# Optimization experiments

Measured on AMD Instinct MI355X. Metric: run time of the kernel, lower is better.

## Reference

```python
import jax, jax.numpy as jnp
import numpy as np

B, S, D, H = 2, 2048, 1024, 16
DK = D // H

def setup_inputs() -> dict:
    key = jax.random.key(0)
    ks = jax.random.split(key, 12)
    s = 1.0 / np.sqrt(D)
    return {
        "q": jax.random.normal(ks[0], (B, S, D), jnp.float32),
        "k": jax.random.normal(ks[1], (B, S, D), jnp.float32),
        "v": jax.random.normal(ks[2], (B, S, D), jnp.float32),
        "mask": jnp.ones((1, 1, S, S), jnp.int32),
        "Wq": jax.random.normal(ks[3], (D, D), jnp.float32) * s,
        "bq": jnp.zeros((D,), jnp.float32),
        "Wk": jax.random.normal(ks[4], (D, D), jnp.float32) * s,
        "bk": jnp.zeros((D,), jnp.float32),
        "Wv": jax.random.normal(ks[5], (D, D), jnp.float32) * s,
        "bv": jnp.zeros((D,), jnp.float32),
        "Wo": jax.random.normal(ks[6], (D, D), jnp.float32) * s,
        "bo": jnp.zeros((D,), jnp.float32),
    }

def reference(q, k, v, mask, Wq, bq, Wk, bk, Wv, bv, Wo, bo):
    # projections (torch Linear: x @ W^T + b)
    Q = q @ Wq.T + bq
    K = k @ Wk.T + bk
    V = v @ Wv.T + bv
    # split heads: [B,S,D] -> [B,H,S,DK]
    def split(x):
        return x.reshape(B, S, H, DK).transpose(0, 2, 1, 3)
    Qh, Kh, Vh = split(Q), split(K), split(V)
    scores = jnp.einsum('bhqd,bhkd->bhqk', Qh, Kh) / jnp.sqrt(jnp.float32(DK))
    scores = jnp.where(mask == 0, jnp.float32(-1e9), scores)
    attn = jax.nn.softmax(scores, axis=-1)  # dropout p=0.0 -> identity
    x = jnp.einsum('bhqk,bhkd->bhqd', attn, Vh)
    x = x.transpose(0, 2, 1, 3).reshape(B, S, D)
    return x @ Wo.T + bo
```

## Files before the change

### kernel.cpp

```cpp
#include <hip/hip_runtime.h>
#include <hip/hip_bf16.h>
#include <stdint.h>

#define B_    2
#define S_    2048
#define D_    1024
#define H_    16
#define NTOK  (B_ * S_)

typedef __attribute__((ext_vector_type(8))) short bf16x8;
typedef __attribute__((ext_vector_type(4))) float f32x4;
typedef __attribute__((ext_vector_type(2))) float float2v;
typedef __attribute__((ext_vector_type(2))) __bf16 bfv2;

static __device__ __forceinline__ unsigned int pkbf(float a, float b) {
    float2v fv = {a, b};
    bfv2 r = __builtin_convertvector(fv, bfv2);
    unsigned int u;
    __builtin_memcpy(&u, &r, 4);
    return u;
}

using g_cu32 = __attribute__((address_space(1))) const unsigned int;
using l_u32  = __attribute__((address_space(3))) unsigned int;
static __device__ __forceinline__ void gld16(const void* g, void* l) {
    __builtin_amdgcn_global_load_lds((g_cu32*)g, (l_u32*)l, 16, 0, 0);
}

template<int N> static __device__ __forceinline__ void wait_vm() {
    if constexpr (N == 0)      asm volatile("s_waitcnt vmcnt(0)" ::: "memory");
    else if constexpr (N == 2) asm volatile("s_waitcnt vmcnt(2)" ::: "memory");
    else if constexpr (N == 3) asm volatile("s_waitcnt vmcnt(3)" ::: "memory");
    else if constexpr (N == 4) asm volatile("s_waitcnt vmcnt(4)" ::: "memory");
}

#define QN ((size_t)NTOK * D_)
#define WN ((size_t)D_ * D_)

struct SwapT { static constexpr bool value = true; };
struct NoSwapT { static constexpr bool value = false; };

__global__ __launch_bounds__(256) void prep_kernel(
    const float* __restrict__ q, const float* __restrict__ k, const float* __restrict__ v,
    const float* __restrict__ Wq, const float* __restrict__ Wk,
    const float* __restrict__ Wv, const float* __restrict__ Wo,
    const int* __restrict__ mask,
    unsigned short* __restrict__ qb, unsigned short* __restrict__ kb,
    unsigned short* __restrict__ vb, unsigned short* __restrict__ wqb,
    unsigned short* __restrict__ wkb, unsigned short* __restrict__ wvb,
    unsigned short* __restrict__ wob, int* __restrict__ flags) {
    __shared__ int anyz;
    if (blockIdx.x < 8192) {
        size_t i = ((size_t)blockIdx.x * 256 + threadIdx.x) * 8;
        const float* s; unsigned short* d; size_t off;
        if (i < QN)          { s = q; d = qb; off = i; }
        else if (i < 2 * QN) { s = k; d = kb; off = i - QN; }
        else if (i < 3 * QN) { s = v; d = vb; off = i - 2 * QN; }
        else {
            size_t j = i - 3 * QN;
            int wi = (int)(j >> 20);
            s = (wi == 0) ? Wq : (wi == 1) ? Wk : (wi == 2) ? Wv : Wo;
            d = (wi == 0) ? wqb : (wi == 1) ? wkb : (wi == 2) ? wvb : wob;
            off = j & (WN - 1);
        }
        float4 a = *(const float4*)(s + off);
        float4 b = *(const float4*)(s + off + 4);
        uint4 pk;
        pk.x = pkbf(a.x, a.y); pk.y = pkbf(a.z, a.w);
        pk.z = pkbf(b.x, b.y); pk.w = pkbf(b.z, b.w);
        *(uint4*)(d + off) = pk;
    } else {
        if (threadIdx.x == 0) anyz = 0;
        __syncthreads();
        int bid2 = blockIdx.x - 8192;
        const int qt = bid2 >> 5, kt = bid2 & 31;
        int az = 0;
        for (int i = threadIdx.x; i < 64 * 64; i += 256) {
            int r = i >> 6, c = i & 63;
            az |= (mask[(size_t)(qt * 64 + r) * S_ + kt * 64 + c] == 0) ? 1 : 0;
        }
        if (az) atomicOr(&anyz, 1);
        __syncthreads();
        if (threadIdx.x == 0) flags[qt * 32 + kt] = anyz;
    }
}

struct GemmArgs {
    const unsigned short* A[3];
    const unsigned short* W[3];
    const float* bias[3];
    void* C[3];
    int mode[3];
    float scale[3];
};

template<int BMT>
__global__ __launch_bounds__(256, 3) void gemm_async(GemmArgs ga) {
    constexpr int AG = BMT / 16;
    constexpr int MI = BMT / 32;
    constexpr int NK = D_ / 32;
    constexpr int LOADS = (BMT == 128) ? 4 : 3;
    const int z = blockIdx.z;
    const unsigned short* __restrict__ A = ga.A[z];
    const unsigned short* __restrict__ W = ga.W[z];
    const float* __restrict__ bias = ga.bias[z];
    void* C = ga.C[z];
    const int mode = ga.mode[z];
    const float scl = ga.scale[z];

    __shared__ unsigned short As[3][AG * 512];
    __shared__ unsigned short Bs[3][8 * 512];

    const int t    = threadIdx.x;
    const int lane = t & 63;
    const int w    = t >> 6;
    const int fr   = lane & 15;
    const int kq   = lane >> 4;
    const int wrow = w >> 1, wcol = w & 1;
    const int m0 = blockIdx.x * BMT, n0 = blockIdx.y * 128;

    const int sc = lane >> 4;
    const int sr = lane & 15;

    const unsigned short* ga0;
    const unsigned short* ga1 = nullptr;
    int la0Off, la1Off = 0;
    if constexpr (BMT == 128) {
        ga0 = A + (size_t)(m0 + (2 * w) * 16 + sr) * D_ + sc * 8;
        ga1 = ga0 + 16 * D_;
        la0Off = (2 * w) * 512;
        la1Off = (2 * w + 1) * 512;
    } else {
        ga0 = A + (size_t)(m0 + w * 16 + sr) * D_ + sc * 8;
        la0Off = w * 512;
    }
    const unsigned short* gw0 = W + (size_t)(n0 + (2 * w) * 16 + sr) * D_ + sc * 8;
    const unsigned short* gw1 = gw0 + 16 * D_;
    const int lw0Off = (2 * w) * 512;
    const int lw1Off = (2 * w + 1) * 512;

    int aOff[MI], bOff[4];
#pragma unroll
    for (int mi = 0; mi < MI; ++mi) aOff[mi] = (wrow * MI + mi) * 512 + (kq * 16 + fr) * 8;
#pragma unroll
    for (int ni = 0; ni < 4; ++ni) bOff[ni] = (wcol * 4 + ni) * 512 + (kq * 16 + fr) * 8;

    f32x4 acc[MI][4];
#pragma unroll
    for (int i = 0; i < MI; ++i)
#pragma unroll
        for (int j = 0; j < 4; ++j) acc[i][j] = (f32x4)0.0f;

    auto stage = [&](int buf) {
        gld16(ga0, &As[buf][la0Off]);
        if constexpr (BMT == 128) gld16(ga1, &As[buf][la1Off]);
        gld16(gw0, &Bs[buf][lw0Off]);
        gld16(gw1, &Bs[buf][lw1Off]);
        ga0 += 32; gw0 += 32; gw1 += 32;
        if constexpr (BMT == 128) ga1 += 32;
    };

    auto kloop = [&](auto swc) {
        constexpr bool SW = decltype(swc)::value;
        auto mma_step = [&](int cur) {
            const unsigned short* Ab = As[cur];
            const unsigned short* Bb = Bs[cur];
            bf16x8 af[MI], bfr[4];
#pragma unroll
            for (int mi = 0; mi < MI; ++mi) af[mi] = *(const bf16x8*)&Ab[aOff[mi]];
#pragma unroll
            for (int ni = 0; ni < 4; ++ni) bfr[ni] = *(const bf16x8*)&Bb[bOff[ni]];
#pragma unroll
            for (int mi = 0; mi < MI; ++mi)
#pragma unroll
                for (int ni = 0; ni < 4; ++ni) {
                    if constexpr (SW)
                        acc[mi][ni] = __builtin_amdgcn_mfma_f32_16x16x32_bf16(
                            bfr[ni], af[mi], acc[mi][ni], 0, 0, 0);
                    else
                        acc[mi][ni] = __builtin_amdgcn_mfma_f32_16x16x32_bf16(
                            af[mi], bfr[ni], acc[mi][ni], 0, 0, 0);
                }
        };

        stage(0);
        stage(1);
        int cur = 0;
        for (int k0 = 0; k0 < NK - 1; ++k0) {
            __builtin_amdgcn_sched_barrier(0);
            wait_vm<LOADS>();
            __builtin_amdgcn_s_barrier();
            __builtin_amdgcn_sched_barrier(0);
            if (k0 + 2 < NK) {
                int pf = (cur >= 1) ? cur - 1 : cur + 2;
                stage(pf);
            }
            mma_step(cur);
            cur = (cur < 2) ? cur + 1 : 0;
        }
        __builtin_amdgcn_sched_barrier(0);
        wait_vm<0>();
        __builtin_amdgcn_s_barrier();
        __builtin_amdgcn_sched_barrier(0);
        mma_step(cur);
    };
    if (mode == 2) kloop(NoSwapT{}); else kloop(SwapT{});

    if (mode == 2) {
        unsigned short* Co = (unsigned short*)C;
#pragma unroll
        for (int ni = 0; ni < 4; ++ni) {
            int col = n0 + wcol * 64 + ni * 16 + fr;
            float bv = bias[col];
            int hh = col >> 6, d = col & 63;
#pragma unroll
            for (int mi = 0; mi < MI; ++mi) {
                int tok = m0 + wrow * (BMT / 2) + mi * 16 + kq * 4;
                int bb = tok >> 11, sbase = tok & (S_ - 1);
                uint2 pk;
                pk.x = pkbf((acc[mi][ni][0] + bv) * scl, (acc[mi][ni][1] + bv) * scl);
                pk.y = pkbf((acc[mi][ni][2] + bv) * scl, (acc[mi][ni][3] + bv) * scl);
                *(uint2*)(Co + ((size_t)((bb * H_ + hh) * 64 + d)) * S_ + sbase) = pk;
            }
        }
    } else if (mode == 0) {
        float* Co = (float*)C;
#pragma unroll
        for (int ni = 0; ni < 4; ++ni) {
            int nb = n0 + wcol * 64 + ni * 16 + kq * 4;
            float4 b4 = *(const float4*)&bias[nb];
#pragma unroll
            for (int mi = 0; mi < MI; ++mi) {
                int m = m0 + wrow * (BMT / 2) + mi * 16 + fr;
                float4 o4;
                o4.x = (acc[mi][ni][0] + b4.x) * scl;
                o4.y = (acc[mi][ni][1] + b4.y) * scl;
                o4.z = (acc[mi][ni][2] + b4.z) * scl;
                o4.w = (acc[mi][ni][3] + b4.w) * scl;
                *(float4*)(Co + (size_t)m * D_ + nb) = o4;
            }
        }
    } else {
        unsigned short* Co = (unsigned short*)C;
#pragma unroll
        for (int ni = 0; ni < 4; ++ni) {
            int nb = n0 + wcol * 64 + ni * 16 + kq * 4;
            float4 b4 = *(const float4*)&bias[nb];
#pragma unroll
            for (int mi = 0; mi < MI; ++mi) {
                int m = m0 + wrow * (BMT / 2) + mi * 16 + fr;
                uint2 pk;
                pk.x = pkbf((acc[mi][ni][0] + b4.x) * scl, (acc[mi][ni][1] + b4.y) * scl);
                pk.y = pkbf((acc[mi][ni][2] + b4.z) * scl, (acc[mi][ni][3] + b4.w) * scl);
                *(uint2*)(Co + (size_t)m * D_ + nb) = pk;
            }
        }
    }
}

__global__ __launch_bounds__(512, 4) void flash4(
    const unsigned short* __restrict__ Qb, const unsigned short* __restrict__ Kb,
    const unsigned short* __restrict__ Vtg, const int* __restrict__ mask,
    const int* __restrict__ flags, unsigned short* __restrict__ Xb) {
    __shared__ unsigned short Ks[3][4096];
    __shared__ unsigned short Vs[3][4096];
    __shared__ unsigned short Ps[8192];

    const int t    = threadIdx.x;
    const int lane = t & 63;
    const int w    = t >> 6;
    const int fr   = lane & 15;
    const int kq   = lane >> 4;
    const int bid = blockIdx.x;
    const int swb = ((bid & 7) << 6) | (bid >> 3);
    const int qt = swb & 15, hd = (swb >> 4) & 15, b = swb >> 8;
    const int q0 = qt * 128;
    const int swz = fr & 7;

    const unsigned short* qrow_p = Qb + (size_t)(b * S_ + q0 + w * 16 + fr) * D_ + hd * 64;
    bf16x8 qf[2];
    qf[0] = *(const bf16x8*)(qrow_p + kq * 8);
    qf[1] = *(const bf16x8*)(qrow_p + 32 + kq * 8);

    int fl = (lane < 32) ? flags[(qt * 2 + (w >> 2)) * 32 + lane] : 0;
    unsigned int fmask = (unsigned int)__ballot(fl != 0);

    const unsigned short* kptr =
        Kb + (size_t)(b * S_ + (w >> 1) * 16 + fr) * D_ + hd * 64 + (w & 1) * 32 + kq * 8;
    const unsigned short* vptr =
        Vtg + ((size_t)((b * H_ + hd) * 64 + (w >> 1) * 16 + fr)) * S_ + (w & 1) * 32 + kq * 8;

    gld16(kptr, (char*)&Ks[0][0] + w * 1024);
    gld16(vptr, (char*)&Vs[0][0] + w * 1024);
    gld16(kptr + (size_t)64 * D_, (char*)&Ks[1][0] + w * 1024);
    gld16(vptr + 64,              (char*)&Vs[1][0] + w * 1024);
    const unsigned short* kpf = kptr + (size_t)128 * D_;
    const unsigned short* vpf = vptr + 128;

    unsigned short* pswr[4];
#pragma unroll
    for (int mi = 0; mi < 4; ++mi) {
        int chunk = mi * 2 + (kq >> 1);
        pswr[mi] = &Ps[(w * 16 + fr) * 64 + ((chunk ^ swz) << 3) + ((kq & 1) << 2)];
    }
    const unsigned short* psrd[2];
#pragma unroll
    for (int kk = 0; kk < 2; ++kk) {
        int c = kk * 4 + kq;
        psrd[kk] = &Ps[(w * 16 + fr) * 64 + ((c ^ swz) << 3)];
    }

    const f32x4 zf = (f32x4)0.0f;
    f32x4 o[4];
#pragma unroll
    for (int i = 0; i < 4; ++i) o[i] = zf;
    float2v l2 = {0.0f, 0.0f};

    auto attn_step = [&](int cur, int kt) {
        f32x4 st[4];
#pragma unroll
        for (int mi = 0; mi < 4; ++mi) {
            bf16x8 a = *(const bf16x8*)&Ks[cur][mi * 1024 + (kq * 16 + fr) * 8];
            st[mi] = __builtin_amdgcn_mfma_f32_16x16x32_bf16(a, qf[0], zf, 0, 0, 0);
        }
#pragma unroll
        for (int mi = 0; mi < 4; ++mi) {
            bf16x8 a = *(const bf16x8*)&Ks[cur][mi * 1024 + ((4 + kq) * 16 + fr) * 8];
            st[mi] = __builtin_amdgcn_mfma_f32_16x16x32_bf16(a, qf[1], st[mi], 0, 0, 0);
        }

        if ((fmask >> kt) & 1u) {
#pragma unroll
            for (int mi = 0; mi < 4; ++mi) {
                int4 mv = *(const int4*)&mask[(size_t)(q0 + w * 16 + fr) * S_ + kt * 64 + mi * 16 + kq * 4];
                if (mv.x == 0) st[mi][0] = -3e8f;
                if (mv.y == 0) st[mi][1] = -3e8f;
                if (mv.z == 0) st[mi][2] = -3e8f;
                if (mv.w == 0) st[mi][3] = -3e8f;
            }
        }

#pragma unroll
        for (int mi = 0; mi < 4; ++mi) {
            float e0 = __builtin_amdgcn_exp2f(st[mi][0]);
            float e1 = __builtin_amdgcn_exp2f(st[mi][1]);
            float e2 = __builtin_amdgcn_exp2f(st[mi][2]);
            float e3 = __builtin_amdgcn_exp2f(st[mi][3]);
            l2 += (float2v){e0, e1} + (float2v){e2, e3};
            uint2 pk;
            pk.x = pkbf(e0, e1);
            pk.y = pkbf(e2, e3);
            *(uint2*)pswr[mi] = pk;
        }

#pragma unroll
        for (int kk = 0; kk < 2; ++kk) {
            bf16x8 pb = *(const bf16x8*)psrd[kk];
#pragma unroll
            for (int mi = 0; mi < 4; ++mi) {
                bf16x8 a = *(const bf16x8*)&Vs[cur][mi * 1024 + ((kk * 4 + kq) * 16 + fr) * 8];
                o[mi] = __builtin_amdgcn_mfma_f32_16x16x32_bf16(a, pb, o[mi], 0, 0, 0);
            }
        }
    };

    int cur = 0;
    for (int kt = 0; kt < 31; ++kt) {
        __builtin_amdgcn_sched_barrier(0);
        wait_vm<2>();
        __builtin_amdgcn_s_barrier();
        __builtin_amdgcn_sched_barrier(0);
        if (kt < 30) {
            int pf = (cur >= 1) ? cur - 1 : cur + 2;
            gld16(kpf, (char*)&Ks[pf][0] + w * 1024);
            gld16(vpf, (char*)&Vs[pf][0] + w * 1024);
            kpf += (size_t)64 * D_;
            vpf += 64;
        }
        attn_step(cur, kt);
        cur = (cur < 2) ? cur + 1 : 0;
    }
    __builtin_amdgcn_sched_barrier(0);
    wait_vm<0>();
    __builtin_amdgcn_s_barrier();
    __builtin_amdgcn_sched_barrier(0);
    attn_step(cur, 31);

    float l_i = l2.x + l2.y;
    l_i += __shfl_xor(l_i, 16, 64);
    l_i += __shfl_xor(l_i, 32, 64);
    float rl = 1.0f / l_i;

#pragma unroll
    for (int mi = 0; mi < 4; ++mi) {
        uint2 pk;
        pk.x = pkbf(o[mi][0] * rl, o[mi][1] * rl);
        pk.y = pkbf(o[mi][2] * rl, o[mi][3] * rl);
        *(uint2*)(Xb + (size_t)(b * S_ + q0 + w * 16 + fr) * D_ + hd * 64 + mi * 16 + kq * 4) = pk;
    }
}

extern "C" void kernel_launch(void* const* d_in, const int* in_sizes, int n_in,
                              void* d_out, int out_size, void* d_ws, size_t ws_size,
                              hipStream_t stream) {
    const float* q    = (const float*)d_in[0];
    const float* k    = (const float*)d_in[1];
    const float* v    = (const float*)d_in[2];
    const int*   mask = (const int*)d_in[3];
    const float* Wq   = (const float*)d_in[4];
    const float* bq   = (const float*)d_in[5];
    const float* Wk   = (const float*)d_in[6];
    const float* bk   = (const float*)d_in[7];
    const float* Wv   = (const float*)d_in[8];
    const float* bv   = (const float*)d_in[9];
    const float* Wo   = (const float*)d_in[10];
    const float* bo   = (const float*)d_in[11];
    float* out = (float*)d_out;

    unsigned short* qb  = (unsigned short*)d_ws;
    unsigned short* kb  = qb + QN;
    unsigned short* vb  = kb + QN;
    unsigned short* Qf  = vb + QN;
    unsigned short* Kf  = Qf + QN;
    unsigned short* Vt  = Kf + QN;
    unsigned short* wqb = Vt + QN;
    unsigned short* wkb = wqb + WN;
    unsigned short* wvb = wkb + WN;
    unsigned short* wob = wvb + WN;
    int* flags = (int*)(wob + WN);

    const float SC = 0.18033688011112042f;

    prep_kernel<<<9216, 256, 0, stream>>>(q, k, v, Wq, Wk, Wv, Wo, mask,
                                          qb, kb, vb, wqb, wkb, wvb, wob, flags);

    GemmArgs g1;
    g1.A[0] = qb;  g1.W[0] = wqb; g1.bias[0] = bq; g1.C[0] = Qf; g1.mode[0] = 1; g1.scale[0] = SC;
    g1.A[1] = kb;  g1.W[1] = wkb; g1.bias[1] = bk; g1.C[1] = Kf; g1.mode[1] = 1; g1.scale[1] = 1.0f;
    g1.A[2] = vb;  g1.W[2] = wvb; g1.bias[2] = bv; g1.C[2] = Vt; g1.mode[2] = 2; g1.scale[2] = 1.0f;
    gemm_async<128><<<dim3(NTOK / 128, D_ / 128, 3), 256, 0, stream>>>(g1);

    flash4<<<dim3((S_ / 128) * H_ * B_, 1, 1), 512, 0, stream>>>(Qf, Kf, Vt, mask, flags, Qf);

    GemmArgs g2;
    g2.A[0] = Qf; g2.W[0] = wob; g2.bias[0] = bo; g2.C[0] = out; g2.mode[0] = 0; g2.scale[0] = 1.0f;
    g2.A[1] = g2.A[2] = nullptr; g2.W[1] = g2.W[2] = nullptr;
    g2.bias[1] = g2.bias[2] = nullptr; g2.C[1] = g2.C[2] = nullptr;
    g2.mode[1] = g2.mode[2] = 0; g2.scale[1] = g2.scale[2] = 1.0f;
    gemm_async<64><<<dim3(NTOK / 64, D_ / 128, 1), 256, 0, stream>>>(g2);
}
```

Measured before the change: 260.6 us.

## Double flash query tile per block and swizzle GEMM block order across XCDs

The attention kernel now processes 256 query rows per block (two 16-row chunks per wave), so each K/V tile loaded into shared memory is reused for twice as many queries. The block count halves and the P buffer doubles, and launch bounds drop to 2 blocks per CU to allow the extra registers. The GEMMs switch to a 1D grid whose block index is remapped so neighbouring tiles land on the same XCD, aiming at better L2 locality. This trades lower occupancy and fewer blocks (256 on a large-CU part) for less K/V traffic.

```diff
diff --git a/kernel.cpp b/kernel.cpp
--- a/kernel.cpp
+++ b/kernel.cpp
@@ -100,7 +100,17 @@
     constexpr int MI = BMT / 32;
     constexpr int NK = D_ / 32;
     constexpr int LOADS = (BMT == 128) ? 4 : 3;
-    const int z = blockIdx.z;
+    constexpr int MT = NTOK / BMT;
+    constexpr int PERZ = MT * 8;
+
+    const int bid = blockIdx.x;
+    const int nb8 = (int)gridDim.x >> 3;
+    const int l = (bid & 7) * nb8 + (bid >> 3);
+    const int z = l / PERZ;
+    const int r = l % PERZ;
+    const int bx = r % MT;
+    const int by = r / MT;
+
     const unsigned short* __restrict__ A = ga.A[z];
     const unsigned short* __restrict__ W = ga.W[z];
     const float* __restrict__ bias = ga.bias[z];
@@ -117,7 +127,7 @@
     const int fr   = lane & 15;
     const int kq   = lane >> 4;
     const int wrow = w >> 1, wcol = w & 1;
-    const int m0 = blockIdx.x * BMT, n0 = blockIdx.y * 128;
+    const int m0 = bx * BMT, n0 = by * 128;
 
     const int sc = lane >> 4;
     const int sr = lane & 15;
@@ -258,13 +268,13 @@
     }
 }
 
-__global__ __launch_bounds__(512, 4) void flash4(
+__global__ __launch_bounds__(512, 2) void flash4(
     const unsigned short* __restrict__ Qb, const unsigned short* __restrict__ Kb,
     const unsigned short* __restrict__ Vtg, const int* __restrict__ mask,
     const int* __restrict__ flags, unsigned short* __restrict__ Xb) {
     __shared__ unsigned short Ks[3][4096];
     __shared__ unsigned short Vs[3][4096];
-    __shared__ unsigned short Ps[8192];
+    __shared__ unsigned short Ps[16384];
 
     const int t    = threadIdx.x;
     const int lane = t & 63;
@@ -272,18 +282,27 @@
     const int fr   = lane & 15;
     const int kq   = lane >> 4;
     const int bid = blockIdx.x;
-    const int swb = ((bid & 7) << 6) | (bid >> 3);
-    const int qt = swb & 15, hd = (swb >> 4) & 15, b = swb >> 8;
-    const int q0 = qt * 128;
+    const int swb = ((bid & 7) << 5) | (bid >> 3);
+    const int qt = swb & 7, hd = (swb >> 3) & 15, b = swb >> 7;
+    const int q0 = qt * 256;
     const int swz = fr & 7;
 
-    const unsigned short* qrow_p = Qb + (size_t)(b * S_ + q0 + w * 16 + fr) * D_ + hd * 64;
-    bf16x8 qf[2];
-    qf[0] = *(const bf16x8*)(qrow_p + kq * 8);
-    qf[1] = *(const bf16x8*)(qrow_p + 32 + kq * 8);
-
-    int fl = (lane < 32) ? flags[(qt * 2 + (w >> 2)) * 32 + lane] : 0;
-    unsigned int fmask = (unsigned int)__ballot(fl != 0);
+    bf16x8 qf[2][2];
+#pragma unroll
+    for (int qc = 0; qc < 2; ++qc) {
+        const unsigned short* qrow_p =
+            Qb + (size_t)(b * S_ + q0 + w * 32 + qc * 16 + fr) * D_ + hd * 64;
+        qf[qc][0] = *(const bf16x8*)(qrow_p + kq * 8);
+        qf[qc][1] = *(const bf16x8*)(qrow_p + 32 + kq * 8);
+    }
+
+    unsigned int fmask[2];
+#pragma unroll
+    for (int qc = 0; qc < 2; ++qc) {
+        int qt64 = qt * 4 + ((2 * w + qc) >> 2);
+        int fl = (lane < 32) ? flags[qt64 * 32 + lane] : 0;
+        fmask[qc] = (unsigned int)__ballot(fl != 0);
+    }
 
     const unsigned short* kptr =
         Kb + (size_t)(b * S_ + (w >> 1) * 16 + fr) * D_ + hd * 64 + (w & 1) * 32 + kq * 8;
@@ -297,69 +316,87 @@
     const unsigned short* kpf = kptr + (size_t)128 * D_;
     const unsigned short* vpf = vptr + 128;
 
-    unsigned short* pswr[4];
-#pragma unroll
-    for (int mi = 0; mi < 4; ++mi) {
-        int chunk = mi * 2 + (kq >> 1);
-        pswr[mi] = &Ps[(w * 16 + fr) * 64 + ((chunk ^ swz) << 3) + ((kq & 1) << 2)];
-    }
-    const unsigned short* psrd[2];
-#pragma unroll
-    for (int kk = 0; kk < 2; ++kk) {
-        int c = kk * 4 + kq;
-        psrd[kk] = &Ps[(w * 16 + fr) * 64 + ((c ^ swz) << 3)];
+    unsigned short* pswr[2][4];
+    const unsigned short* psrd[2][2];
+#pragma unroll
+    for (int qc = 0; qc < 2; ++qc) {
+        int row = w * 32 + qc * 16 + fr;
+#pragma unroll
+        for (int mi = 0; mi < 4; ++mi) {
+            int chunk = mi * 2 + (kq >> 1);
+            pswr[qc][mi] = &Ps[row * 64 + ((chunk ^ swz) << 3) + ((kq & 1) << 2)];
+        }
+#pragma unroll
+        for (int kk = 0; kk < 2; ++kk) {
+            int c = kk * 4 + kq;
+            psrd[qc][kk] = &Ps[row * 64 + ((c ^ swz) << 3)];
+        }
     }
 
     const f32x4 zf = (f32x4)0.0f;
-    f32x4 o[4];
-#pragma unroll
-    for (int i = 0; i < 4; ++i) o[i] = zf;
-    float2v l2 = {0.0f, 0.0f};
+    f32x4 o[2][4];
+#pragma unroll
+    for (int qc = 0; qc < 2; ++qc)
+#pragma unroll
+        for (int i = 0; i < 4; ++i) o[qc][i] = zf;
+    float2v l2[2];
+    l2[0] = (float2v){0.0f, 0.0f};
+    l2[1] = (float2v){0.0f, 0.0f};
 
     auto attn_step = [&](int cur, int kt) {
-        f32x4 st[4];
+        f32x4 st[2][4];
 #pragma unroll
         for (int mi = 0; mi < 4; ++mi) {
             bf16x8 a = *(const bf16x8*)&Ks[cur][mi * 1024 + (kq * 16 + fr) * 8];
-            st[mi] = __builtin_amdgcn_mfma_f32_16x16x32_bf16(a, qf[0], zf, 0, 0, 0);
+            st[0][mi] = __builtin_amdgcn_mfma_f32_16x16x32_bf16(a, qf[0][0], zf, 0, 0, 0);
+            st[1][mi] = __builtin_amdgcn_mfma_f32_16x16x32_bf16(a, qf[1][0], zf, 0, 0, 0);
         }
 #pragma unroll
         for (int mi = 0; mi < 4; ++mi) {
             bf16x8 a = *(const bf16x8*)&Ks[cur][mi * 1024 + ((4 + kq) * 16 + fr) * 8];
-            st[mi] = __builtin_amdgcn_mfma_f32_16x16x32_bf16(a, qf[1], st[mi], 0, 0, 0);
-        }
-
-        if ((fmask >> kt) & 1u) {
+            st[0][mi] = __builtin_amdgcn_mfma_f32_16x16x32_bf16(a, qf[0][1], st[0][mi], 0, 0, 0);
+            st[1][mi] = __builtin_amdgcn_mfma_f32_16x16x32_bf16(a, qf[1][1], st[1][mi], 0, 0, 0);
+        }
+
+#pragma unroll
+        for (int qc = 0; qc < 2; ++qc) {
+            if ((fmask[qc] >> kt) & 1u) {
+#pragma unroll
+                for (int mi = 0; mi < 4; ++mi) {
+                    int4 mv = *(const int4*)&mask[(size_t)(q0 + w * 32 + qc * 16 + fr) * S_ +
+                                                  kt * 64 + mi * 16 + kq * 4];
+                    if (mv.x == 0) st[qc][mi][0] = -3e8f;
+                    if (mv.y == 0) st[qc][mi][1] = -3e8f;
+                    if (mv.z == 0) st[qc][mi][2] = -3e8f;
+                    if (mv.w == 0) st[qc][mi][3] = -3e8f;
+                }
+            }
+        }
+
+#pragma unroll
+        for (int qc = 0; qc < 2; ++qc)
 #pragma unroll
             for (int mi = 0; mi < 4; ++mi) {
-                int4 mv = *(const int4*)&mask[(size_t)(q0 + w * 16 + fr) * S_ + kt * 64 + mi * 16 + kq * 4];
-                if (mv.x == 0) st[mi][0] = -3e8f;
-                if (mv.y == 0) st[mi][1] = -3e8f;
-                if (mv.z == 0) st[mi][2] = -3e8f;
-                if (mv.w == 0) st[mi][3] = -3e8f;
-            }
-        }
-
-#pragma unroll
-        for (int mi = 0; mi < 4; ++mi) {
-            float e0 = __builtin_amdgcn_exp2f(st[mi][0]);
-            float e1 = __builtin_amdgcn_exp2f(st[mi][1]);
-            float e2 = __builtin_amdgcn_exp2f(st[mi][2]);
-            float e3 = __builtin_amdgcn_exp2f(st[mi][3]);
-            l2 += (float2v){e0, e1} + (float2v){e2, e3};
-            uint2 pk;
-            pk.x = pkbf(e0, e1);
-            pk.y = pkbf(e2, e3);
-            *(uint2*)pswr[mi] = pk;
-        }
+                float e0 = __builtin_amdgcn_exp2f(st[qc][mi][0]);
+                float e1 = __builtin_amdgcn_exp2f(st[qc][mi][1]);
+                float e2 = __builtin_amdgcn_exp2f(st[qc][mi][2]);
+                float e3 = __builtin_amdgcn_exp2f(st[qc][mi][3]);
+                l2[qc] += (float2v){e0, e1} + (float2v){e2, e3};
+                uint2 pk;
+                pk.x = pkbf(e0, e1);
+                pk.y = pkbf(e2, e3);
+                *(uint2*)pswr[qc][mi] = pk;
+            }
 
 #pragma unroll
         for (int kk = 0; kk < 2; ++kk) {
-            bf16x8 pb = *(const bf16x8*)psrd[kk];
+            bf16x8 pb0 = *(const bf16x8*)psrd[0][kk];
+            bf16x8 pb1 = *(const bf16x8*)psrd[1][kk];
 #pragma unroll
             for (int mi = 0; mi < 4; ++mi) {
                 bf16x8 a = *(const bf16x8*)&Vs[cur][mi * 1024 + ((kk * 4 + kq) * 16 + fr) * 8];
-                o[mi] = __builtin_amdgcn_mfma_f32_16x16x32_bf16(a, pb, o[mi], 0, 0, 0);
+                o[0][mi] = __builtin_amdgcn_mfma_f32_16x16x32_bf16(a, pb0, o[0][mi], 0, 0, 0);
+                o[1][mi] = __builtin_amdgcn_mfma_f32_16x16x32_bf16(a, pb1, o[1][mi], 0, 0, 0);
             }
         }
     };
@@ -386,17 +423,20 @@
     __builtin_amdgcn_sched_barrier(0);
     attn_step(cur, 31);
 
-    float l_i = l2.x + l2.y;
-    l_i += __shfl_xor(l_i, 16, 64);
-    l_i += __shfl_xor(l_i, 32, 64);
-    float rl = 1.0f / l_i;
-
-#pragma unroll
-    for (int mi = 0; mi < 4; ++mi) {
-        uint2 pk;
-        pk.x = pkbf(o[mi][0] * rl, o[mi][1] * rl);
-        pk.y = pkbf(o[mi][2] * rl, o[mi][3] * rl);
-        *(uint2*)(Xb + (size_t)(b * S_ + q0 + w * 16 + fr) * D_ + hd * 64 + mi * 16 + kq * 4) = pk;
+#pragma unroll
+    for (int qc = 0; qc < 2; ++qc) {
+        float l_i = l2[qc].x + l2[qc].y;
+        l_i += __shfl_xor(l_i, 16, 64);
+        l_i += __shfl_xor(l_i, 32, 64);
+        float rl = 1.0f / l_i;
+#pragma unroll
+        for (int mi = 0; mi < 4; ++mi) {
+            uint2 pk;
+            pk.x = pkbf(o[qc][mi][0] * rl, o[qc][mi][1] * rl);
+            pk.y = pkbf(o[qc][mi][2] * rl, o[qc][mi][3] * rl);
+            *(uint2*)(Xb + (size_t)(b * S_ + q0 + w * 32 + qc * 16 + fr) * D_ +
+                      hd * 64 + mi * 16 + kq * 4) = pk;
+        }
     }
 }
 
@@ -438,14 +478,14 @@
     g1.A[0] = qb;  g1.W[0] = wqb; g1.bias[0] = bq; g1.C[0] = Qf; g1.mode[0] = 1; g1.scale[0] = SC;
     g1.A[1] = kb;  g1.W[1] = wkb; g1.bias[1] = bk; g1.C[1] = Kf; g1.mode[1] = 1; g1.scale[1] = 1.0f;
     g1.A[2] = vb;  g1.W[2] = wvb; g1.bias[2] = bv; g1.C[2] = Vt; g1.mode[2] = 2; g1.scale[2] = 1.0f;
-    gemm_async<128><<<dim3(NTOK / 128, D_ / 128, 3), 256, 0, stream>>>(g1);
-
-    flash4<<<dim3((S_ / 128) * H_ * B_, 1, 1), 512, 0, stream>>>(Qf, Kf, Vt, mask, flags, Qf);
+    gemm_async<128><<<768, 256, 0, stream>>>(g1);
+
+    flash4<<<256, 512, 0, stream>>>(Qf, Kf, Vt, mask, flags, Qf);
 
     GemmArgs g2;
     g2.A[0] = Qf; g2.W[0] = wob; g2.bias[0] = bo; g2.C[0] = out; g2.mode[0] = 0; g2.scale[0] = 1.0f;
     g2.A[1] = g2.A[2] = nullptr; g2.W[1] = g2.W[2] = nullptr;
     g2.bias[1] = g2.bias[2] = nullptr; g2.C[1] = g2.C[2] = nullptr;
     g2.mode[1] = g2.mode[2] = 0; g2.scale[1] = g2.scale[2] = 1.0f;
-    gemm_async<64><<<dim3(NTOK / 64, D_ / 128, 1), 256, 0, stream>>>(g2);
-}
+    gemm_async<64><<<512, 256, 0, stream>>>(g2);
+}
```

Result: slower. 266.7 us (+2.3%).
